# Performance work log

Hardware: AMD Instinct MI355X
Metric: run time of the kernel (lower is better)

Reference implementation:

```python
import jax, jax.numpy as jnp
import numpy as np

MAX_DISP = 4  # displacement range [-4, 4] -> 9x9 = 81 output channels


def setup_inputs() -> dict:
    key = jax.random.key(0)
    k1, k2 = jax.random.split(key)
    B, C, H, W = 8, 128, 128, 256
    tensorFirst = jax.random.normal(k1, (B, C, H, W), dtype=jnp.float32)
    tensorSecond = jax.random.normal(k2, (B, C, H, W), dtype=jnp.float32)
    return {"tensorFirst": tensorFirst, "tensorSecond": tensorSecond}


def reference(tensorFirst, tensorSecond):
    # PWC-Net style correlation: out[b, d, y, x] =
    #   (1/C) * sum_c first[b,c,y,x] * second[b,c,y+dy,x+dx]
    # with zero padding, dy,dx in [-4,4], d = (dy+4)*9 + (dx+4).
    B, C, H, W = tensorFirst.shape
    p = MAX_DISP
    second_pad = jnp.pad(tensorSecond, ((0, 0), (0, 0), (p, p), (p, p)))
    outs = []
    for dy in range(-p, p + 1):
        for dx in range(-p, p + 1):
            shifted = jax.lax.dynamic_slice(
                second_pad, (0, 0, dy + p, dx + p), (B, C, H, W))
            # mean over channels, matching the cupy kernel's /C normalization
            outs.append(jnp.mean(tensorFirst * shifted, axis=1))
    return jnp.stack(outs, axis=1)  # [B, 81, H, W]
```

## Files before the change

kernel.cpp:

```cpp
#include <hip/hip_runtime.h>

#define CC   128
#define HH   128
#define WW   256
#define BB   8
#define HWS  (HH * WW)
#define TH   16
#define TW   64
#define SROWS (TH + 8)
#define SCOLS (TW + 8)
#define STILE (SROWS * SCOLS)
#define NTHR 768

typedef float f4 __attribute__((ext_vector_type(4)));

__global__ __launch_bounds__(NTHR)
void corr_kernel(const float* __restrict__ first,
                 const float* __restrict__ second,
                 float* __restrict__ out)
{
    __shared__ float s_lds[2 * STILE];

    const int tid = threadIdx.x;
    const int g   = tid >> 8;
    const int p   = tid & 255;
    const int r   = p >> 4;
    const int xq  = p & 15;
    const int x0  = xq << 2;

    const int bx = blockIdx.x * TW;
    const int by = blockIdx.y * TH;
    const int b  = blockIdx.z;

    const int y  = by + r;
    const int xg = bx + x0;

    const int i0 = tid;
    const int i1 = tid + NTHR;
    const int i2 = tid + 2 * NTHR;

    const int sr0 = i0 / SCOLS, sc0 = i0 % SCOLS;
    const int sr1 = i1 / SCOLS, sc1 = i1 % SCOLS;
    const int sr2 = i2 / SCOLS, sc2 = i2 % SCOLS;

    const int ys0 = by - 4 + sr0, xs0 = bx - 4 + sc0;
    const int ys1 = by - 4 + sr1, xs1 = bx - 4 + sc1;
    const int ys2 = by - 4 + sr2, xs2 = bx - 4 + sc2;

    const bool v0 = ((unsigned)ys0 < HH) && ((unsigned)xs0 < WW);
    const bool v1 = ((unsigned)ys1 < HH) && ((unsigned)xs1 < WW);
    const bool v2 = (i2 < STILE) && ((unsigned)ys2 < HH) && ((unsigned)xs2 < WW);

    const float* sbase = second + (long)b * CC * HWS;
    int go0 = v0 ? (ys0 * WW + xs0) : 0;
    int go1 = v1 ? (ys1 * WW + xs1) : 0;
    int go2 = v2 ? (ys2 * WW + xs2) : 0;

    float acc[3][9][4];
    #pragma unroll
    for (int a = 0; a < 3; ++a)
        #pragma unroll
        for (int d = 0; d < 9; ++d)
            #pragma unroll
            for (int q = 0; q < 4; ++q)
                acc[a][d][q] = 0.0f;

    {
        float t0 = v0 ? sbase[go0] : 0.0f;
        float t1 = v1 ? sbase[go1] : 0.0f;
        float t2 = v2 ? sbase[go2] : 0.0f;
        s_lds[i0] = t0;
        s_lds[i1] = t1;
        if (i2 < STILE) s_lds[i2] = t2;
    }
    __syncthreads();

    const float* fptr = first + ((long)(b * CC) * HH + y) * WW + xg;

    int cur = 0;
    for (int c = 0; c < CC; ++c) {
        float t0 = 0.0f, t1 = 0.0f, t2 = 0.0f;
        const bool more = (c + 1 < CC);
        if (more) {
            const float* sb = sbase + (c + 1) * HWS;
            t0 = v0 ? sb[go0] : 0.0f;
            t1 = v1 ? sb[go1] : 0.0f;
            t2 = v2 ? sb[go2] : 0.0f;
        }

        f4 fv = *(const f4*)fptr;
        fptr += HWS;

        const float* sb_lds = &s_lds[cur * STILE];
        #pragma unroll
        for (int r3 = 0; r3 < 3; ++r3) {
            const int srow = r + g * 3 + r3;
            const f4* wp = (const f4*)&sb_lds[srow * SCOLS + x0];
            f4 wa = wp[0];
            f4 wb = wp[1];
            f4 wc = wp[2];
            float w[12];
            w[0] = wa[0]; w[1]  = wa[1]; w[2]  = wa[2]; w[3]  = wa[3];
            w[4] = wb[0]; w[5]  = wb[1]; w[6]  = wb[2]; w[7]  = wb[3];
            w[8] = wc[0]; w[9]  = wc[1]; w[10] = wc[2]; w[11] = wc[3];
            #pragma unroll
            for (int dxi = 0; dxi < 9; ++dxi) {
                #pragma unroll
                for (int px = 0; px < 4; ++px) {
                    acc[r3][dxi][px] = fmaf(fv[px], w[dxi + px], acc[r3][dxi][px]);
                }
            }
        }

        if (more) {
            const int nb = (cur ^ 1) * STILE;
            s_lds[nb + i0] = t0;
            s_lds[nb + i1] = t1;
            if (i2 < STILE) s_lds[nb + i2] = t2;
        }
        __syncthreads();
        cur ^= 1;
    }

    const float scale = 1.0f / (float)CC;
    #pragma unroll
    for (int r3 = 0; r3 < 3; ++r3) {
        #pragma unroll
        for (int dxi = 0; dxi < 9; ++dxi) {
            const int d = (g * 3 + r3) * 9 + dxi;
            f4 o;
            o[0] = acc[r3][dxi][0] * scale;
            o[1] = acc[r3][dxi][1] * scale;
            o[2] = acc[r3][dxi][2] * scale;
            o[3] = acc[r3][dxi][3] * scale;
            *(f4*)(out + (long)(b * 81 + d) * HWS + y * WW + xg) = o;
        }
    }
}

extern "C" void kernel_launch(void* const* d_in, const int* in_sizes, int n_in,
                              void* d_out, int out_size, void* d_ws, size_t ws_size,
                              hipStream_t stream) {
    const float* first  = (const float*)d_in[0];
    const float* second = (const float*)d_in[1];
    float* out = (float*)d_out;

    dim3 grid(WW / TW, HH / TH, BB);
    corr_kernel<<<grid, NTHR, 0, stream>>>(first, second, out);
}
```

Before: 160.2 us.

## Halve tile width, stage two channels per barrier, raise occupancy target

Shrinks the spatial tile from 64 to 32 columns and the block from 768 to 384 threads, and stages two channels of the shifted halo tile per double-buffered iteration so there is half as many __syncthreads. Launch bounds now request 3 blocks per CU to improve latency hiding. The cost is a larger halo overhead ratio (40 vs 32 columns loaded per 32 outputs), so more redundant global/LDS traffic, and more prefetch registers per thread.

```diff
diff --git a/kernel.cpp b/kernel.cpp
--- a/kernel.cpp
+++ b/kernel.cpp
@@ -6,26 +6,28 @@
 #define BB   8
 #define HWS  (HH * WW)
 #define TH   16
-#define TW   64
+#define TW   32
 #define SROWS (TH + 8)
 #define SCOLS (TW + 8)
 #define STILE (SROWS * SCOLS)
-#define NTHR 768
+#define NTHR 384
+#define CPI  2
+#define STG  ((CPI * STILE) / NTHR)
 
 typedef float f4 __attribute__((ext_vector_type(4)));
 
-__global__ __launch_bounds__(NTHR)
+__global__ __launch_bounds__(NTHR, 3)
 void corr_kernel(const float* __restrict__ first,
                  const float* __restrict__ second,
                  float* __restrict__ out)
 {
-    __shared__ float s_lds[2 * STILE];
+    __shared__ float s_lds[2 * CPI * STILE];
 
     const int tid = threadIdx.x;
-    const int g   = tid >> 8;
-    const int p   = tid & 255;
-    const int r   = p >> 4;
-    const int xq  = p & 15;
+    const int g   = tid >> 7;
+    const int p   = tid & 127;
+    const int r   = p >> 3;
+    const int xq  = p & 7;
     const int x0  = xq << 2;
 
     const int bx = blockIdx.x * TW;
@@ -35,26 +37,24 @@
     const int y  = by + r;
     const int xg = bx + x0;
 
-    const int i0 = tid;
-    const int i1 = tid + NTHR;
-    const int i2 = tid + 2 * NTHR;
-
-    const int sr0 = i0 / SCOLS, sc0 = i0 % SCOLS;
-    const int sr1 = i1 / SCOLS, sc1 = i1 % SCOLS;
-    const int sr2 = i2 / SCOLS, sc2 = i2 % SCOLS;
-
-    const int ys0 = by - 4 + sr0, xs0 = bx - 4 + sc0;
-    const int ys1 = by - 4 + sr1, xs1 = bx - 4 + sc1;
-    const int ys2 = by - 4 + sr2, xs2 = bx - 4 + sc2;
-
-    const bool v0 = ((unsigned)ys0 < HH) && ((unsigned)xs0 < WW);
-    const bool v1 = ((unsigned)ys1 < HH) && ((unsigned)xs1 < WW);
-    const bool v2 = (i2 < STILE) && ((unsigned)ys2 < HH) && ((unsigned)xs2 < WW);
+    int  goff[STG];
+    int  lidx[STG];
+    bool val[STG];
+    #pragma unroll
+    for (int k = 0; k < STG; ++k) {
+        const int i   = tid + k * NTHR;
+        const int ch  = i / STILE;
+        const int idx = i - ch * STILE;
+        const int sr  = idx / SCOLS;
+        const int sc  = idx - sr * SCOLS;
+        const int ys  = by - 4 + sr;
+        const int xs  = bx - 4 + sc;
+        val[k]  = ((unsigned)ys < HH) && ((unsigned)xs < WW);
+        goff[k] = val[k] ? (ch * HWS + ys * WW + xs) : 0;
+        lidx[k] = i;
+    }
 
     const float* sbase = second + (long)b * CC * HWS;
-    int go0 = v0 ? (ys0 * WW + xs0) : 0;
-    int go1 = v1 ? (ys1 * WW + xs1) : 0;
-    int go2 = v2 ? (ys2 * WW + xs2) : 0;
 
     float acc[3][9][4];
     #pragma unroll
@@ -65,58 +65,61 @@
             for (int q = 0; q < 4; ++q)
                 acc[a][d][q] = 0.0f;
 
-    {
-        float t0 = v0 ? sbase[go0] : 0.0f;
-        float t1 = v1 ? sbase[go1] : 0.0f;
-        float t2 = v2 ? sbase[go2] : 0.0f;
-        s_lds[i0] = t0;
-        s_lds[i1] = t1;
-        if (i2 < STILE) s_lds[i2] = t2;
+    #pragma unroll
+    for (int k = 0; k < STG; ++k) {
+        float t = val[k] ? sbase[goff[k]] : 0.0f;
+        s_lds[lidx[k]] = t;
     }
     __syncthreads();
 
     const float* fptr = first + ((long)(b * CC) * HH + y) * WW + xg;
 
     int cur = 0;
-    for (int c = 0; c < CC; ++c) {
-        float t0 = 0.0f, t1 = 0.0f, t2 = 0.0f;
-        const bool more = (c + 1 < CC);
+    const int NIT = CC / CPI;
+    for (int it = 0; it < NIT; ++it) {
+        float t[STG];
+        const bool more = (it + 1 < NIT);
         if (more) {
-            const float* sb = sbase + (c + 1) * HWS;
-            t0 = v0 ? sb[go0] : 0.0f;
-            t1 = v1 ? sb[go1] : 0.0f;
-            t2 = v2 ? sb[go2] : 0.0f;
+            const float* sb = sbase + (it + 1) * (CPI * HWS);
+            #pragma unroll
+            for (int k = 0; k < STG; ++k)
+                t[k] = val[k] ? sb[goff[k]] : 0.0f;
         }
 
-        f4 fv = *(const f4*)fptr;
-        fptr += HWS;
+        f4 fv0 = *(const f4*)fptr;
+        f4 fv1 = *(const f4*)(fptr + HWS);
+        fptr += CPI * HWS;
 
-        const float* sb_lds = &s_lds[cur * STILE];
         #pragma unroll
-        for (int r3 = 0; r3 < 3; ++r3) {
-            const int srow = r + g * 3 + r3;
-            const f4* wp = (const f4*)&sb_lds[srow * SCOLS + x0];
-            f4 wa = wp[0];
-            f4 wb = wp[1];
-            f4 wc = wp[2];
-            float w[12];
-            w[0] = wa[0]; w[1]  = wa[1]; w[2]  = wa[2]; w[3]  = wa[3];
-            w[4] = wb[0]; w[5]  = wb[1]; w[6]  = wb[2]; w[7]  = wb[3];
-            w[8] = wc[0]; w[9]  = wc[1]; w[10] = wc[2]; w[11] = wc[3];
+        for (int cc = 0; cc < CPI; ++cc) {
+            const float* sb_lds = &s_lds[cur * (CPI * STILE) + cc * STILE];
+            const f4 fv = (cc == 0) ? fv0 : fv1;
             #pragma unroll
-            for (int dxi = 0; dxi < 9; ++dxi) {
+            for (int r3 = 0; r3 < 3; ++r3) {
+                const int srow = r + g * 3 + r3;
+                const f4* wp = (const f4*)&sb_lds[srow * SCOLS + x0];
+                f4 wa = wp[0];
+                f4 wb = wp[1];
+                f4 wc = wp[2];
+                float w[12];
+                w[0] = wa[0]; w[1]  = wa[1]; w[2]  = wa[2]; w[3]  = wa[3];
+                w[4] = wb[0]; w[5]  = wb[1]; w[6]  = wb[2]; w[7]  = wb[3];
+                w[8] = wc[0]; w[9]  = wc[1]; w[10] = wc[2]; w[11] = wc[3];
                 #pragma unroll
-                for (int px = 0; px < 4; ++px) {
-                    acc[r3][dxi][px] = fmaf(fv[px], w[dxi + px], acc[r3][dxi][px]);
+                for (int dxi = 0; dxi < 9; ++dxi) {
+                    #pragma unroll
+                    for (int px = 0; px < 4; ++px) {
+                        acc[r3][dxi][px] = fmaf(fv[px], w[dxi + px], acc[r3][dxi][px]);
+                    }
                 }
             }
         }
 
         if (more) {
-            const int nb = (cur ^ 1) * STILE;
-            s_lds[nb + i0] = t0;
-            s_lds[nb + i1] = t1;
-            if (i2 < STILE) s_lds[nb + i2] = t2;
+            const int nb = (cur ^ 1) * (CPI * STILE);
+            #pragma unroll
+            for (int k = 0; k < STG; ++k)
+                s_lds[nb + lidx[k]] = t[k];
         }
         __syncthreads();
         cur ^= 1;
```

Result: slower. 436.2 us (+172.3%).

## Shrink tiles, pack channel pairs as fp16 in LDS, deepen prefetch

Applied to the files above, without the earlier changes.

Shrinks the spatial tile to 16x16 with 576 threads, where each thread owns one displacement row (9 outputs x 4 pixels), cutting the accumulators per thread and raising occupancy (launch bounds min 5 blocks). The second-image tile is stored in LDS as two channels packed into one fp16x2 word, halving LDS traffic and the number of barriers per channel. A two-stage register prefetch of the second tensor is added. The fp16 rounding of the second input lowers precision relative to the fp32 reference, and smaller tiles increase halo reloads from global memory.

```diff
diff --git a/kernel.cpp b/kernel.cpp
--- a/kernel.cpp
+++ b/kernel.cpp
@@ -6,27 +6,29 @@
 #define BB   8
 #define HWS  (HH * WW)
 #define TH   16
-#define TW   64
-#define SROWS (TH + 8)
-#define SCOLS (TW + 8)
-#define STILE (SROWS * SCOLS)
-#define NTHR 768
+#define TW   16
+#define SR   (TH + 8)
+#define SC   (TW + 8)
+#define ST   (SR * SC)
+#define NTHR 576
+#define NPAIR (CC / 2)
 
-typedef float f4 __attribute__((ext_vector_type(4)));
+typedef float    f4 __attribute__((ext_vector_type(4)));
+typedef unsigned u4 __attribute__((ext_vector_type(4)));
+typedef __fp16   h2 __attribute__((ext_vector_type(2)));
 
-__global__ __launch_bounds__(NTHR)
+__global__ __launch_bounds__(NTHR, 5)
 void corr_kernel(const float* __restrict__ first,
                  const float* __restrict__ second,
                  float* __restrict__ out)
 {
-    __shared__ float s_lds[2 * STILE];
+    __shared__ __align__(16) unsigned s_lds[2 * ST];
 
     const int tid = threadIdx.x;
-    const int g   = tid >> 8;
-    const int p   = tid & 255;
-    const int r   = p >> 4;
-    const int xq  = p & 15;
-    const int x0  = xq << 2;
+    const int g   = tid >> 6;
+    const int l   = tid & 63;
+    const int r   = l >> 2;
+    const int x0  = (l & 3) << 2;
 
     const int bx = blockIdx.x * TW;
     const int by = blockIdx.y * TH;
@@ -35,106 +37,86 @@
     const int y  = by + r;
     const int xg = bx + x0;
 
-    const int i0 = tid;
-    const int i1 = tid + NTHR;
-    const int i2 = tid + 2 * NTHR;
+    const int sr = tid / SC, sc = tid % SC;
+    const int ys = by - 4 + sr, xs = bx - 4 + sc;
+    const bool v = ((unsigned)ys < HH) && ((unsigned)xs < WW);
+    const float* sp = second + (long)b * CC * HWS + (v ? (ys * WW + xs) : 0);
 
-    const int sr0 = i0 / SCOLS, sc0 = i0 % SCOLS;
-    const int sr1 = i1 / SCOLS, sc1 = i1 % SCOLS;
-    const int sr2 = i2 / SCOLS, sc2 = i2 % SCOLS;
+    float acc[9][4];
+    #pragma unroll
+    for (int d = 0; d < 9; ++d)
+        #pragma unroll
+        for (int q = 0; q < 4; ++q)
+            acc[d][q] = 0.0f;
 
-    const int ys0 = by - 4 + sr0, xs0 = bx - 4 + sc0;
-    const int ys1 = by - 4 + sr1, xs1 = bx - 4 + sc1;
-    const int ys2 = by - 4 + sr2, xs2 = bx - 4 + sc2;
-
-    const bool v0 = ((unsigned)ys0 < HH) && ((unsigned)xs0 < WW);
-    const bool v1 = ((unsigned)ys1 < HH) && ((unsigned)xs1 < WW);
-    const bool v2 = (i2 < STILE) && ((unsigned)ys2 < HH) && ((unsigned)xs2 < WW);
-
-    const float* sbase = second + (long)b * CC * HWS;
-    int go0 = v0 ? (ys0 * WW + xs0) : 0;
-    int go1 = v1 ? (ys1 * WW + xs1) : 0;
-    int go2 = v2 ? (ys2 * WW + xs2) : 0;
-
-    float acc[3][9][4];
-    #pragma unroll
-    for (int a = 0; a < 3; ++a)
-        #pragma unroll
-        for (int d = 0; d < 9; ++d)
-            #pragma unroll
-            for (int q = 0; q < 4; ++q)
-                acc[a][d][q] = 0.0f;
-
+    float p1a, p1b;
     {
-        float t0 = v0 ? sbase[go0] : 0.0f;
-        float t1 = v1 ? sbase[go1] : 0.0f;
-        float t2 = v2 ? sbase[go2] : 0.0f;
-        s_lds[i0] = t0;
-        s_lds[i1] = t1;
-        if (i2 < STILE) s_lds[i2] = t2;
+        float a0 = v ? sp[0]   : 0.0f;
+        float b0 = v ? sp[HWS] : 0.0f;
+        h2 pk = __builtin_amdgcn_cvt_pkrtz(a0, b0);
+        s_lds[tid] = __builtin_bit_cast(unsigned, pk);
+        p1a = v ? sp[2 * (long)HWS] : 0.0f;
+        p1b = v ? sp[3 * (long)HWS] : 0.0f;
     }
     __syncthreads();
 
-    const float* fptr = first + ((long)(b * CC) * HH + y) * WW + xg;
+    const float* fp = first + (long)b * CC * HWS + (long)y * WW + xg;
 
     int cur = 0;
-    for (int c = 0; c < CC; ++c) {
-        float t0 = 0.0f, t1 = 0.0f, t2 = 0.0f;
-        const bool more = (c + 1 < CC);
-        if (more) {
-            const float* sb = sbase + (c + 1) * HWS;
-            t0 = v0 ? sb[go0] : 0.0f;
-            t1 = v1 ? sb[go1] : 0.0f;
-            t2 = v2 ? sb[go2] : 0.0f;
+    for (int it = 0; it < NPAIR; ++it) {
+        float p2a = 0.0f, p2b = 0.0f;
+        if (it + 2 < NPAIR) {
+            const float* s2 = sp + (long)(2 * (it + 2)) * HWS;
+            p2a = v ? s2[0]   : 0.0f;
+            p2b = v ? s2[HWS] : 0.0f;
         }
 
-        f4 fv = *(const f4*)fptr;
-        fptr += HWS;
+        const unsigned* wrow = &s_lds[cur * ST + (r + g) * SC + x0];
+        u4 wa = *(const u4*)wrow;
+        u4 wb = *(const u4*)(wrow + 4);
+        u4 wc = *(const u4*)(wrow + 8);
+        unsigned wu[12] = { wa[0], wa[1], wa[2], wa[3],
+                            wb[0], wb[1], wb[2], wb[3],
+                            wc[0], wc[1], wc[2], wc[3] };
+        float w0[12], w1[12];
+        #pragma unroll
+        for (int j = 0; j < 12; ++j) {
+            h2 hv = __builtin_bit_cast(h2, wu[j]);
+            w0[j] = (float)hv[0];
+            w1[j] = (float)hv[1];
+        }
 
-        const float* sb_lds = &s_lds[cur * STILE];
+        f4 f0 = *(const f4*)fp;
+        f4 f1 = *(const f4*)(fp + HWS);
+        fp += 2 * HWS;
+
         #pragma unroll
-        for (int r3 = 0; r3 < 3; ++r3) {
-            const int srow = r + g * 3 + r3;
-            const f4* wp = (const f4*)&sb_lds[srow * SCOLS + x0];
-            f4 wa = wp[0];
-            f4 wb = wp[1];
-            f4 wc = wp[2];
-            float w[12];
-            w[0] = wa[0]; w[1]  = wa[1]; w[2]  = wa[2]; w[3]  = wa[3];
-            w[4] = wb[0]; w[5]  = wb[1]; w[6]  = wb[2]; w[7]  = wb[3];
-            w[8] = wc[0]; w[9]  = wc[1]; w[10] = wc[2]; w[11] = wc[3];
+        for (int dxi = 0; dxi < 9; ++dxi) {
             #pragma unroll
-            for (int dxi = 0; dxi < 9; ++dxi) {
-                #pragma unroll
-                for (int px = 0; px < 4; ++px) {
-                    acc[r3][dxi][px] = fmaf(fv[px], w[dxi + px], acc[r3][dxi][px]);
-                }
+            for (int px = 0; px < 4; ++px) {
+                acc[dxi][px] = fmaf(f1[px], w1[dxi + px],
+                               fmaf(f0[px], w0[dxi + px], acc[dxi][px]));
             }
         }
 
-        if (more) {
-            const int nb = (cur ^ 1) * STILE;
-            s_lds[nb + i0] = t0;
-            s_lds[nb + i1] = t1;
-            if (i2 < STILE) s_lds[nb + i2] = t2;
+        if (it + 1 < NPAIR) {
+            h2 pk = __builtin_amdgcn_cvt_pkrtz(p1a, p1b);
+            s_lds[(cur ^ 1) * ST + tid] = __builtin_bit_cast(unsigned, pk);
         }
         __syncthreads();
+        p1a = p2a; p1b = p2b;
         cur ^= 1;
     }
 
     const float scale = 1.0f / (float)CC;
     #pragma unroll
-    for (int r3 = 0; r3 < 3; ++r3) {
-        #pragma unroll
-        for (int dxi = 0; dxi < 9; ++dxi) {
-            const int d = (g * 3 + r3) * 9 + dxi;
-            f4 o;
-            o[0] = acc[r3][dxi][0] * scale;
-            o[1] = acc[r3][dxi][1] * scale;
-            o[2] = acc[r3][dxi][2] * scale;
-            o[3] = acc[r3][dxi][3] * scale;
-            *(f4*)(out + (long)(b * 81 + d) * HWS + y * WW + xg) = o;
-        }
+    for (int dxi = 0; dxi < 9; ++dxi) {
+        f4 o;
+        o[0] = acc[dxi][0] * scale;
+        o[1] = acc[dxi][1] * scale;
+        o[2] = acc[dxi][2] * scale;
+        o[3] = acc[dxi][3] * scale;
+        *(f4*)(out + ((long)(b * 81 + g * 9 + dxi)) * HWS + (long)y * WW + xg) = o;
     }
 }
 
```

Measured after the change: 363.7 us. +127.1%, slower.

## Prefetch second tile two channels ahead and relax barrier to LDS-only wait

Applied to the files above, without the earlier changes.

Global loads of the second tensor are now issued two channels ahead and held in registers, and the first-tensor vector is prefetched one channel ahead. The LDS write of the next tile moves to the top of each iteration, before the compute. __syncthreads is replaced with an lgkmcnt-only wait plus s_barrier, so outstanding global loads no longer stall at the barrier. This gives more memory latency hiding at the cost of extra live registers in a 768-thread block. The final iterations redundantly reload the last channel, which is harmless.

```diff
diff --git a/kernel.cpp b/kernel.cpp
--- a/kernel.cpp
+++ b/kernel.cpp
@@ -52,9 +52,9 @@
     const bool v2 = (i2 < STILE) && ((unsigned)ys2 < HH) && ((unsigned)xs2 < WW);
 
     const float* sbase = second + (long)b * CC * HWS;
-    int go0 = v0 ? (ys0 * WW + xs0) : 0;
-    int go1 = v1 ? (ys1 * WW + xs1) : 0;
-    int go2 = v2 ? (ys2 * WW + xs2) : 0;
+    const int go0 = v0 ? (ys0 * WW + xs0) : 0;
+    const int go1 = v1 ? (ys1 * WW + xs1) : 0;
+    const int go2 = v2 ? (ys2 * WW + xs2) : 0;
 
     float acc[3][9][4];
     #pragma unroll
@@ -66,30 +66,42 @@
                 acc[a][d][q] = 0.0f;
 
     {
-        float t0 = v0 ? sbase[go0] : 0.0f;
-        float t1 = v1 ? sbase[go1] : 0.0f;
-        float t2 = v2 ? sbase[go2] : 0.0f;
-        s_lds[i0] = t0;
-        s_lds[i1] = t1;
-        if (i2 < STILE) s_lds[i2] = t2;
+        float a0 = v0 ? sbase[go0] : 0.0f;
+        float a1 = v1 ? sbase[go1] : 0.0f;
+        float a2 = v2 ? sbase[go2] : 0.0f;
+        s_lds[i0] = a0;
+        s_lds[i1] = a1;
+        if (i2 < STILE) s_lds[i2] = a2;
     }
-    __syncthreads();
+    float t1a = v0 ? sbase[HWS + go0] : 0.0f;
+    float t1b = v1 ? sbase[HWS + go1] : 0.0f;
+    float t1c = v2 ? sbase[HWS + go2] : 0.0f;
 
     const float* fptr = first + ((long)(b * CC) * HH + y) * WW + xg;
+    f4 fv = *(const f4*)fptr;
+    fptr += HWS;
+
+    asm volatile("s_waitcnt lgkmcnt(0)" ::: "memory");
+    __builtin_amdgcn_s_barrier();
 
     int cur = 0;
-    for (int c = 0; c < CC; ++c) {
-        float t0 = 0.0f, t1 = 0.0f, t2 = 0.0f;
-        const bool more = (c + 1 < CC);
-        if (more) {
-            const float* sb = sbase + (c + 1) * HWS;
-            t0 = v0 ? sb[go0] : 0.0f;
-            t1 = v1 ? sb[go1] : 0.0f;
-            t2 = v2 ? sb[go2] : 0.0f;
-        }
+    #pragma unroll 2
+    for (int it = 0; it < CC; ++it) {
+        const bool more2 = (it + 2 < CC);
 
-        f4 fv = *(const f4*)fptr;
-        fptr += HWS;
+        const int c2 = more2 ? (it + 2) : it;
+        const float* sb2 = sbase + (long)c2 * HWS;
+        float t2a = v0 ? sb2[go0] : 0.0f;
+        float t2b = v1 ? sb2[go1] : 0.0f;
+        float t2c = v2 ? sb2[go2] : 0.0f;
+
+        f4 fnx = *(const f4*)fptr;
+        fptr += more2 ? HWS : 0;
+
+        const int nb = (cur ^ 1) * STILE;
+        s_lds[nb + i0] = t1a;
+        s_lds[nb + i1] = t1b;
+        if (i2 < STILE) s_lds[nb + i2] = t1c;
 
         const float* sb_lds = &s_lds[cur * STILE];
         #pragma unroll
@@ -99,10 +111,9 @@
             f4 wa = wp[0];
             f4 wb = wp[1];
             f4 wc = wp[2];
-            float w[12];
-            w[0] = wa[0]; w[1]  = wa[1]; w[2]  = wa[2]; w[3]  = wa[3];
-            w[4] = wb[0]; w[5]  = wb[1]; w[6]  = wb[2]; w[7]  = wb[3];
-            w[8] = wc[0]; w[9]  = wc[1]; w[10] = wc[2]; w[11] = wc[3];
+            float w[12] = { wa[0], wa[1], wa[2], wa[3],
+                            wb[0], wb[1], wb[2], wb[3],
+                            wc[0], wc[1], wc[2], wc[3] };
             #pragma unroll
             for (int dxi = 0; dxi < 9; ++dxi) {
                 #pragma unroll
@@ -112,13 +123,11 @@
             }
         }
 
-        if (more) {
-            const int nb = (cur ^ 1) * STILE;
-            s_lds[nb + i0] = t0;
-            s_lds[nb + i1] = t1;
-            if (i2 < STILE) s_lds[nb + i2] = t2;
-        }
-        __syncthreads();
+        asm volatile("s_waitcnt lgkmcnt(0)" ::: "memory");
+        __builtin_amdgcn_s_barrier();
+
+        t1a = t2a; t1b = t2b; t1c = t2c;
+        fv = fnx;
         cur ^= 1;
     }
 
```

Result: slower. 206.3 us (+28.8%).
